# Performance work log

Measured on AMD Instinct MI355X. Metric: run time of the kernel, lower is better.

## Reference

```python
import jax, jax.numpy as jnp
import numpy as np

B = 32768
NM = 3      # number of modalities (len(mk))
NE = 8      # number of experts
D_IN = 768
D_P = 128   # per-modality projection dim
D_X = D_P * NM  # 384, concatenated feature dim


def setup_inputs() -> dict:
    key = jax.random.key(0)
    ks = jax.random.split(key, 16)
    s = 0.02
    return {
        "feat_text": jax.random.normal(ks[0], (B, D_IN), jnp.float32),
        "feat_audio": jax.random.normal(ks[1], (B, D_IN), jnp.float32),
        "feat_video": jax.random.normal(ks[2], (B, D_IN), jnp.float32),
        "proj_w": jax.random.normal(ks[3], (NM, D_IN, D_P), jnp.float32) * s,
        "proj_b": jax.random.normal(ks[4], (NM, D_P), jnp.float32) * s,
        "exp_w1": jax.random.normal(ks[5], (NE, D_X, D_P), jnp.float32) * s,
        "exp_b1": jax.random.normal(ks[6], (NE, D_P), jnp.float32) * s,
        "exp_w2": jax.random.normal(ks[7], (NE, D_P, D_P), jnp.float32) * s,
        "exp_b2": jax.random.normal(ks[8], (NE, D_P), jnp.float32) * s,
        "gate_w": jax.random.normal(ks[9], (D_X, NE), jnp.float32) * s,
        "gate_b": jax.random.normal(ks[10], (NE,), jnp.float32) * s,
        "pre_w": jax.random.normal(ks[11], (D_P, 64), jnp.float32) * s,
        "pre_b": jax.random.normal(ks[12], (64,), jnp.float32) * s,
        "head_w": jax.random.normal(ks[13], (64, 2), jnp.float32) * s,
        "head_b": jax.random.normal(ks[14], (2,), jnp.float32) * s,
    }


def reference(feat_text, feat_audio, feat_video, proj_w, proj_b,
              exp_w1, exp_b1, exp_w2, exp_b2, gate_w, gate_b,
              pre_w, pre_b, head_w, head_b):
    feats = jnp.stack([feat_text, feat_audio, feat_video], axis=0)  # [M,B,768]
    # per-modality projections, then concat: [B, 128*M]
    proj = jnp.einsum('mbd,mdp->mbp', feats, proj_w) + proj_b[:, None, :]
    x = jnp.concatenate(jnp.split(proj, NM, axis=0), axis=-1)[0]  # [B, 384]
    # gate: softmax over 8 experts
    gw = jax.nn.softmax(x @ gate_w + gate_b, axis=-1)  # [B, 8]
    # all experts as batched GEMM: [E,B,128]
    h = jax.nn.relu(jnp.einsum('bx,exh->ebh', x, exp_w1) + exp_b1[:, None, :])
    eo = jnp.einsum('ebh,eho->ebo', h, exp_w2) + exp_b2[:, None, :]
    fused = jnp.einsum('be,ebh->bh', gw, eo)  # weighted sum over experts
    penult = jax.nn.relu(fused @ pre_w + pre_b)  # Dropout is identity in eval
    logits = penult @ head_w + head_b  # [B, 2]
    return logits
```

## Files before the change

kernel.cpp:

```cpp
#include <hip/hip_runtime.h>
#include <hip/hip_bf16.h>

#define B_ROWS 32768

typedef unsigned short u16;
typedef unsigned int u32;
typedef float f32x4 __attribute__((ext_vector_type(4)));
typedef __bf16 bf16x8 __attribute__((ext_vector_type(8)));

__device__ __forceinline__ u16 f2bf(float f){
    union { float f; u32 u; } v; v.f = f;
    return (u16)((v.u + 0x7FFFu + ((v.u >> 16) & 1u)) >> 16);
}
__device__ __forceinline__ float bf2f(u16 h){
    union { u32 u; float f; } v; v.u = ((u32)h) << 16; return v.f;
}
__device__ __forceinline__ u32 cvtpk(float lo, float hi){
    u32 r;
    asm("v_cvt_pk_bf16_f32 %0, %1, %2" : "=v"(r) : "v"(lo), "v"(hi));
    return r;
}
__device__ __forceinline__ void async_cp16(void* lds_dst, const void* g_src){
    __builtin_amdgcn_global_load_lds(
        (const __attribute__((address_space(1))) unsigned int*)g_src,
        (__attribute__((address_space(3))) unsigned int*)lds_dst, 16, 0, 0);
}

__global__ void cast_weights_kernel(const float* __restrict__ proj_w,
                                    const float* __restrict__ exp_w1,
                                    const float* __restrict__ exp_w2,
                                    const float* __restrict__ pre_w,
                                    const float* __restrict__ gate_w,
                                    u16* __restrict__ pimg, u16* __restrict__ w1img,
                                    u16* __restrict__ w2img, u16* __restrict__ prwT,
                                    u16* __restrict__ gwimg){
    int i = blockIdx.x * 256 + threadIdx.x;
    if (i < 294912){
        int m = i / 98304, r = i % 98304;
        int c = r / 4096, rr = r % 4096;
        int col = rr >> 5, kk = rr & 31;
        int kb = kk ^ (((col >> 1) & 3) << 3);
        pimg[i] = f2bf(proj_w[m*98304 + (c*32 + kb)*128 + col]);
    } else if (i < 688128){
        int j = i - 294912;
        int e = j / 49152, r = j % 49152;
        int ph = r / 4096, rr = r % 4096;
        int q = rr >> 10, col = (rr >> 3) & 127, el = rr & 7;
        w1img[j] = f2bf(exp_w1[e*49152 + (ph*32 + q*8 + el)*128 + col]);
    } else if (i < 819200){
        int j = i - 688128;
        int e = j / 16384, r = j % 16384;
        int c2 = r / 4096, rr = r % 4096;
        int q = rr >> 10, col = (rr >> 3) & 127, el = rr & 7;
        w2img[j] = f2bf(exp_w2[e*16384 + (c2*32 + q*8 + el)*128 + col]);
    } else if (i < 827392){
        int j = i - 819200;
        int o = j / 128, k = j % 128;
        prwT[j] = f2bf(pre_w[k*64 + o]);
    } else if (i < 833536){
        int j = i - 827392;
        int e = j / 384, k = j % 384;
        gwimg[j] = (e < 8) ? f2bf(gate_w[k*8 + e]) : (u16)0;
    }
}

#define XS_OFF   0
#define ST_OFF   98304
#define WB_OFF   98304
#define HS_OFF   114688
#define GWT_OFF  149504
#define B1_OFF   153600
#define B2_OFF   155648

__global__ __launch_bounds__(512, 2) void fused_kernel(
    const float* __restrict__ ft, const float* __restrict__ fa, const float* __restrict__ fv,
    const u16* __restrict__ pimg, const float* __restrict__ proj_b,
    const u16* __restrict__ w1img, const u16* __restrict__ w2img,
    const u16* __restrict__ prwT, const u16* __restrict__ gwimg,
    const float* __restrict__ gate_b, const float* __restrict__ exp_b1, const float* __restrict__ exp_b2,
    const float* __restrict__ pre_b, const float* __restrict__ head_w, const float* __restrict__ head_b,
    float* __restrict__ out)
{
    __shared__ __align__(16) char lds[157696];
    const int tid = threadIdx.x;
    const int lane = tid & 63, wid = tid >> 6;
    const int wr = wid >> 1, wc = wid & 1;
    const int lr = lane & 15, q = lane >> 4;
    const int blk = blockIdx.x;
    const int row0 = blk * 128;
    const char* w1b = (const char*)w1img;
    const char* w2b = (const char*)w2img;
    u16* Hs  = (u16*)(lds + HS_OFF);
    u16* b1L = (u16*)(lds + B1_OFF);
    u16* b2L = (u16*)(lds + B2_OFF);

    if (tid < 384) ((float*)(lds + GWT_OFF))[tid] = proj_b[tid];
    for (int i = tid; i < 1024; i += 512){
        b1L[i] = f2bf(exp_b1[i]);
        b2L[i] = f2bf(exp_b2[i]);
    }
    asm volatile("s_waitcnt vmcnt(0)" ::: "memory");

    u32 aoffs[2];
    #pragma unroll
    for (int i = 0; i < 2; i++){
        int P = i*8192 + tid*16;
        int row = P >> 7, inner = P & 127;
        aoffs[i] = (u32)((row0 + row)*3072 + (inner ^ ((row & 7) << 4)));
    }

#define PSTAGE(s, c) do{                                                       \
        int mm = (c) / 24, kk = (c) % 24;                                      \
        const float* fb = (mm == 0) ? ft : (mm == 1) ? fa : fv;                \
        const char* ab = (const char*)fb;                                      \
        char* la = lds + ST_OFF + (s)*24576 + tid*16;                          \
        async_cp16(la,        ab + aoffs[0] + kk*128);                         \
        async_cp16(la + 8192, ab + aoffs[1] + kk*128);                         \
        async_cp16(lds + ST_OFF + (s)*24576 + 16384 + tid*16,                  \
                   (const char*)pimg + mm*196608 + kk*8192 + tid*16);          \
    }while(0)

#define PCONSUME(s) do{                                                        \
        const char* Abuf = lds + ST_OFF + (s)*24576;                           \
        const char* Bbuf = Abuf + 16384;                                       \
        bf16x8 af[2];                                                          \
        _Pragma("unroll")                                                      \
        for (int mi = 0; mi < 2; mi++){                                        \
            int row = wr*32 + mi*16 + lr;                                      \
            int aoff = row*128 + ((q*32) ^ ((row & 7) << 4));                  \
            f32x4 a0 = *(const f32x4*)(Abuf + aoff);                           \
            f32x4 a1 = *(const f32x4*)(Abuf + (aoff ^ 16));                    \
            union { u32 w[4]; bf16x8 v; } u;                                   \
            u.w[0] = cvtpk(a0.x, a0.y); u.w[1] = cvtpk(a0.z, a0.w);            \
            u.w[2] = cvtpk(a1.x, a1.y); u.w[3] = cvtpk(a1.z, a1.w);            \
            af[mi] = u.v;                                                      \
        }                                                                      \
        _Pragma("unroll")                                                      \
        for (int ni = 0; ni < 4; ni++){                                        \
            int col = wc*64 + ni*16 + lr;                                      \
            int boff = col*64 + ((q*16) ^ (((col >> 1) & 3) << 4));            \
            bf16x8 bf = *(const bf16x8*)(Bbuf + boff);                         \
            acc[0][ni] = __builtin_amdgcn_mfma_f32_16x16x32_bf16(af[0], bf, acc[0][ni], 0, 0, 0); \
            acc[1][ni] = __builtin_amdgcn_mfma_f32_16x16x32_bf16(af[1], bf, acc[1][ni], 0, 0, 0); \
        }                                                                      \
    }while(0)

    f32x4 acc[2][4];
    #pragma unroll
    for (int i = 0; i < 2; i++)
        #pragma unroll
        for (int j = 0; j < 4; j++) acc[i][j] = {0.f, 0.f, 0.f, 0.f};

    PSTAGE(0, 0);
    int cur = 0;
    #pragma unroll 1
    for (int m = 0; m < 3; m++){
        #pragma unroll 1
        for (int kt = 0; kt < 24; kt++){
            int t = m*24 + kt;
            __builtin_amdgcn_sched_barrier(0);
            __builtin_amdgcn_s_barrier();
            if (t < 71){
                PSTAGE(cur ^ 1, t + 1);
                asm volatile("s_waitcnt vmcnt(3)" ::: "memory");
            } else {
                asm volatile("s_waitcnt vmcnt(0)" ::: "memory");
            }
            __builtin_amdgcn_s_barrier();
            __builtin_amdgcn_sched_barrier(0);
            PCONSUME(cur);
            cur ^= 1;
        }
        const float* pbL = (const float*)(lds + GWT_OFF);
        #pragma unroll
        for (int mi = 0; mi < 2; mi++)
            #pragma unroll
            for (int ni = 0; ni < 4; ni++){
                int lcol = wc*64 + ni*16 + lr;
                int colg = m*128 + lcol;
                int ktI = colg >> 5, qI = (colg >> 3) & 3, el = colg & 7;
                float bias = pbL[m*128 + lcol];
                #pragma unroll
                for (int j = 0; j < 4; j++){
                    int row = wr*32 + mi*16 + q*4 + j;
                    *(u16*)(lds + (row >> 6)*49152 + ktI*4096 + qI*1024
                            + (row & 63)*16 + el*2) = f2bf(acc[mi][ni][j] + bias);
                    acc[mi][ni][j] = 0.f;
                }
            }
    }
#undef PSTAGE
#undef PCONSUME
    asm volatile("s_waitcnt lgkmcnt(0)" ::: "memory");
    __builtin_amdgcn_sched_barrier(0);
    __builtin_amdgcn_s_barrier();

    async_cp16(lds + WB_OFF + tid*16, w1b + tid*16);

    {
        f32x4 ga = {0.f, 0.f, 0.f, 0.f};
        const char* xb = lds + (wid >> 2)*49152 + ((wid & 3)*16 + lr)*16 + q*1024;
        const u16* gwp = gwimg + lr*384 + q*8;
        #pragma unroll
        for (int kt = 0; kt < 12; kt++){
            bf16x8 af = *(const bf16x8*)(xb + kt*4096);
            bf16x8 gb = *(const bf16x8*)(gwp + kt*32);
            ga = __builtin_amdgcn_mfma_f32_16x16x32_bf16(af, gb, ga, 0, 0, 0);
        }
        float gbv = gate_b[lr & 7];
        float gw4[4];
        #pragma unroll
        for (int j = 0; j < 4; j++){
            float v = ga[j] + gbv;
            float mx = v;
            mx = fmaxf(mx, __shfl_xor(mx, 1));
            mx = fmaxf(mx, __shfl_xor(mx, 2));
            mx = fmaxf(mx, __shfl_xor(mx, 4));
            float s = __expf(v - mx);
            float t = s;
            t += __shfl_xor(t, 1);
            t += __shfl_xor(t, 2);
            t += __shfl_xor(t, 4);
            gw4[j] = s / t;
        }
        __builtin_amdgcn_s_barrier();
        if (lr < 8){
            f32x4 wv = {gw4[0], gw4[1], gw4[2], gw4[3]};
            *(f32x4*)(lds + GWT_OFF + lr*512 + (wid*16 + q*4)*4) = wv;
        }
    }
    asm volatile("s_waitcnt vmcnt(0) lgkmcnt(0)" ::: "memory");
    __builtin_amdgcn_sched_barrier(0);
    __builtin_amdgcn_s_barrier();

    f32x4 fus[2][4];
    #pragma unroll
    for (int i = 0; i < 2; i++)
        #pragma unroll
        for (int j = 0; j < 4; j++) fus[i][j] = {0.f, 0.f, 0.f, 0.f};
    cur = 0;

    #pragma unroll 1
    for (int e = 0; e < 8; e++){
        f32x4 ac1[2][4];
        #pragma unroll
        for (int i = 0; i < 2; i++)
            #pragma unroll
            for (int j = 0; j < 4; j++) ac1[i][j] = {0.f, 0.f, 0.f, 0.f};

        #pragma unroll 1
        for (int ph = 0; ph < 12; ph++){
            __builtin_amdgcn_sched_barrier(0);
            __builtin_amdgcn_s_barrier();
            {
                int gn = e*16 + ph + 1;
                int en = gn >> 4, pn = gn & 15;
                const char* src = (pn < 12) ? (w1b + en*98304 + pn*8192)
                                            : (w2b + en*32768 + (pn - 12)*8192);
                async_cp16(lds + WB_OFF + (cur ^ 1)*8192 + tid*16, src + tid*16);
            }
            asm volatile("s_waitcnt vmcnt(1)" ::: "memory");
            __builtin_amdgcn_s_barrier();
            __builtin_amdgcn_sched_barrier(0);
            const char* wsl = lds + WB_OFF + cur*8192 + q*2048;
            const char* xa  = lds + (wr >> 1)*49152 + ph*4096 + q*1024;
            bf16x8 af0 = *(const bf16x8*)(xa + ((wr & 1)*32 + lr)*16);
            bf16x8 af1 = *(const bf16x8*)(xa + ((wr & 1)*32 + 16 + lr)*16);
            #pragma unroll
            for (int ni = 0; ni < 4; ni++){
                bf16x8 bf = *(const bf16x8*)(wsl + (wc*64 + ni*16 + lr)*16);
                ac1[0][ni] = __builtin_amdgcn_mfma_f32_16x16x32_bf16(af0, bf, ac1[0][ni], 0, 0, 0);
                ac1[1][ni] = __builtin_amdgcn_mfma_f32_16x16x32_bf16(af1, bf, ac1[1][ni], 0, 0, 0);
            }
            cur ^= 1;
        }
        #pragma unroll
        for (int mi = 0; mi < 2; mi++)
            #pragma unroll
            for (int ni = 0; ni < 4; ni++){
                int col = wc*64 + ni*16 + lr;
                float b1v = bf2f(b1L[e*128 + col]);
                #pragma unroll
                for (int j = 0; j < 4; j++){
                    int row = wr*32 + mi*16 + q*4 + j;
                    Hs[row*136 + col] = f2bf(fmaxf(ac1[mi][ni][j] + b1v, 0.f));
                }
            }
        asm volatile("s_waitcnt lgkmcnt(0)" ::: "memory");
        __builtin_amdgcn_sched_barrier(0);

        f32x4 ac2[2][4];
        #pragma unroll
        for (int i = 0; i < 2; i++)
            #pragma unroll
            for (int j = 0; j < 4; j++) ac2[i][j] = {0.f, 0.f, 0.f, 0.f};

        #pragma unroll 1
        for (int p2 = 0; p2 < 4; p2++){
            __builtin_amdgcn_sched_barrier(0);
            __builtin_amdgcn_s_barrier();
            {
                int gn = e*16 + 13 + p2;
                if (gn > 127) gn = 127;
                int en = gn >> 4, pn = gn & 15;
                const char* src = (pn < 12) ? (w1b + en*98304 + pn*8192)
                                            : (w2b + en*32768 + (pn - 12)*8192);
                async_cp16(lds + WB_OFF + (cur ^ 1)*8192 + tid*16, src + tid*16);
            }
            asm volatile("s_waitcnt vmcnt(1)" ::: "memory");
            __builtin_amdgcn_s_barrier();
            __builtin_amdgcn_sched_barrier(0);
            const char* wsl = lds + WB_OFF + cur*8192 + q*2048;
            const char* hb  = (const char*)Hs + (p2*32 + q*8)*2;
            bf16x8 af0 = *(const bf16x8*)(hb + (wr*32 + lr)*272);
            bf16x8 af1 = *(const bf16x8*)(hb + (wr*32 + 16 + lr)*272);
            #pragma unroll
            for (int ni = 0; ni < 4; ni++){
                bf16x8 bf = *(const bf16x8*)(wsl + (wc*64 + ni*16 + lr)*16);
                ac2[0][ni] = __builtin_amdgcn_mfma_f32_16x16x32_bf16(af0, bf, ac2[0][ni], 0, 0, 0);
                ac2[1][ni] = __builtin_amdgcn_mfma_f32_16x16x32_bf16(af1, bf, ac2[1][ni], 0, 0, 0);
            }
            cur ^= 1;
        }
        #pragma unroll
        for (int mi = 0; mi < 2; mi++){
            f32x4 gwv = *(const f32x4*)(lds + GWT_OFF + e*512 + (wr*32 + mi*16 + q*4)*4);
            #pragma unroll
            for (int ni = 0; ni < 4; ni++){
                int col = wc*64 + ni*16 + lr;
                float b2v = bf2f(b2L[e*128 + col]);
                #pragma unroll
                for (int j = 0; j < 4; j++)
                    fus[mi][ni][j] += gwv[j] * (ac2[mi][ni][j] + b2v);
            }
        }
    }

    asm volatile("s_waitcnt vmcnt(0)" ::: "memory");
    __builtin_amdgcn_sched_barrier(0);
    __builtin_amdgcn_s_barrier();
    #pragma unroll
    for (int mi = 0; mi < 2; mi++)
        #pragma unroll
        for (int ni = 0; ni < 4; ni++){
            int col = wc*64 + ni*16 + lr;
            #pragma unroll
            for (int j = 0; j < 4; j++){
                int row = wr*32 + mi*16 + q*4 + j;
                Hs[row*136 + col] = f2bf(fus[mi][ni][j]);
            }
        }
    asm volatile("s_waitcnt lgkmcnt(0)" ::: "memory");
    __builtin_amdgcn_sched_barrier(0);
    __builtin_amdgcn_s_barrier();

    f32x4 ap[4];
    #pragma unroll
    for (int i = 0; i < 4; i++) ap[i] = {0.f, 0.f, 0.f, 0.f};
    #pragma unroll
    for (int kt = 0; kt < 4; kt++){
        bf16x8 af = *(const bf16x8*)((const char*)Hs + (wid*16 + lr)*272 + (kt*32 + q*8)*2);
        #pragma unroll
        for (int ni = 0; ni < 4; ni++){
            bf16x8 bf = *(const bf16x8*)(prwT + (size_t)(ni*16 + lr)*128 + kt*32 + q*8);
            ap[ni] = __builtin_amdgcn_mfma_f32_16x16x32_bf16(af, bf, ap[ni], 0, 0, 0);
        }
    }
    float* Pen = (float*)lds;
    #pragma unroll
    for (int ni = 0; ni < 4; ni++){
        int col = ni*16 + lr;
        float pbv = pre_b[col];
        #pragma unroll
        for (int j = 0; j < 4; j++){
            int row = wid*16 + q*4 + j;
            Pen[row*68 + col] = fmaxf(ap[ni][j] + pbv, 0.f);
        }
    }
    asm volatile("s_waitcnt lgkmcnt(0)" ::: "memory");
    __builtin_amdgcn_sched_barrier(0);
    __builtin_amdgcn_s_barrier();
    if (tid < 256){
        int r = tid >> 1, c = tid & 1;
        float s = head_b[c];
        #pragma unroll 8
        for (int k = 0; k < 64; k++) s += Pen[r*68 + k] * head_w[k*2 + c];
        out[(size_t)(blk*128 + r)*2 + c] = s;
    }
}

extern "C" void kernel_launch(void* const* d_in, const int* in_sizes, int n_in,
                              void* d_out, int out_size, void* d_ws, size_t ws_size,
                              hipStream_t stream) {
    const float* ft     = (const float*)d_in[0];
    const float* fa     = (const float*)d_in[1];
    const float* fv     = (const float*)d_in[2];
    const float* proj_w = (const float*)d_in[3];
    const float* proj_b = (const float*)d_in[4];
    const float* exp_w1 = (const float*)d_in[5];
    const float* exp_b1 = (const float*)d_in[6];
    const float* exp_w2 = (const float*)d_in[7];
    const float* exp_b2 = (const float*)d_in[8];
    const float* gate_w = (const float*)d_in[9];
    const float* gate_b = (const float*)d_in[10];
    const float* pre_w  = (const float*)d_in[11];
    const float* pre_b  = (const float*)d_in[12];
    const float* head_w = (const float*)d_in[13];
    const float* head_b = (const float*)d_in[14];
    float* out = (float*)d_out;

    u16* pimg  = (u16*)d_ws;
    u16* w1img = pimg + 294912;
    u16* w2img = w1img + 393216;
    u16* prwT  = w2img + 131072;
    u16* gwimg = prwT + 8192;

    cast_weights_kernel<<<3256, 256, 0, stream>>>(proj_w, exp_w1, exp_w2, pre_w, gate_w,
                                                  pimg, w1img, w2img, prwT, gwimg);
    fused_kernel<<<256, 512, 0, stream>>>(ft, fa, fv, pimg, proj_b,
                                          w1img, w2img, prwT, gwimg,
                                          gate_b, exp_b1, exp_b2,
                                          pre_b, head_w, head_b, out);
}
```

Measured before the change: 122.6 us.

## Deepen async load pipelines to three stages and swizzle hidden-activation LDS layout

The projection GEMM now uses separate A and B staging buffers, with a triple-buffered A ring prefetched two steps ahead and a double-buffered B ring. The expert-weight stream is triple-buffered with a two-ahead prefetch, waiting on vmcnt(2) instead of vmcnt(1). The hidden-activation buffer switches from a padded 136-element stride to an XOR-swizzled 256-byte stride, and projection biases move into registers. LDS use grows to 160 KB, which may limit occupancy despite launch_bounds(512,2).

```diff
diff --git a/kernel.cpp b/kernel.cpp
--- a/kernel.cpp
+++ b/kernel.cpp
@@ -65,12 +65,13 @@
 }
 
 #define XS_OFF   0
-#define ST_OFF   98304
-#define WB_OFF   98304
-#define HS_OFF   114688
-#define GWT_OFF  149504
-#define B1_OFF   153600
-#define B2_OFF   155648
+#define A_OFF    98304
+#define B_OFF    147456
+#define HS_OFF   98304
+#define GWT_OFF  131072
+#define B1_OFF   135168
+#define B2_OFF   137216
+#define WB_OFF   139264
 
 __global__ __launch_bounds__(512, 2) void fused_kernel(
     const float* __restrict__ ft, const float* __restrict__ fa, const float* __restrict__ fv,
@@ -81,7 +82,7 @@
     const float* __restrict__ pre_b, const float* __restrict__ head_w, const float* __restrict__ head_b,
     float* __restrict__ out)
 {
-    __shared__ __align__(16) char lds[157696];
+    __shared__ __align__(16) char lds[163840];
     const int tid = threadIdx.x;
     const int lane = tid & 63, wid = tid >> 6;
     const int wr = wid >> 1, wc = wid & 1;
@@ -90,14 +91,17 @@
     const int row0 = blk * 128;
     const char* w1b = (const char*)w1img;
     const char* w2b = (const char*)w2img;
-    u16* Hs  = (u16*)(lds + HS_OFF);
+    char* HsB = lds + HS_OFF;
     u16* b1L = (u16*)(lds + B1_OFF);
     u16* b2L = (u16*)(lds + B2_OFF);
 
-    if (tid < 384) ((float*)(lds + GWT_OFF))[tid] = proj_b[tid];
-    for (int i = tid; i < 1024; i += 512){
-        b1L[i] = f2bf(exp_b1[i]);
-        b2L[i] = f2bf(exp_b2[i]);
+    float pb0[4], pb1[4], pb2[4];
+    #pragma unroll
+    for (int ni = 0; ni < 4; ni++){
+        int c = wc*64 + ni*16 + lr;
+        pb0[ni] = proj_b[c];
+        pb1[ni] = proj_b[128 + c];
+        pb2[ni] = proj_b[256 + c];
     }
     asm volatile("s_waitcnt vmcnt(0)" ::: "memory");
 
@@ -109,20 +113,23 @@
         aoffs[i] = (u32)((row0 + row)*3072 + (inner ^ ((row & 7) << 4)));
     }
 
-#define PSTAGE(s, c) do{                                                       \
-        int mm = (c) / 24, kk = (c) % 24;                                      \
-        const float* fb = (mm == 0) ? ft : (mm == 1) ? fa : fv;                \
-        const char* ab = (const char*)fb;                                      \
-        char* la = lds + ST_OFF + (s)*24576 + tid*16;                          \
-        async_cp16(la,        ab + aoffs[0] + kk*128);                         \
-        async_cp16(la + 8192, ab + aoffs[1] + kk*128);                         \
-        async_cp16(lds + ST_OFF + (s)*24576 + 16384 + tid*16,                  \
-                   (const char*)pimg + mm*196608 + kk*8192 + tid*16);          \
+#define ASTAGE(c) do{                                                          \
+        int mm_ = (c) / 24, kk_ = (c) % 24;                                    \
+        const char* ab_ = (const char*)(mm_ == 0 ? ft : mm_ == 1 ? fa : fv);   \
+        char* la_ = lds + A_OFF + ((c) % 3)*16384 + tid*16;                    \
+        async_cp16(la_,        ab_ + aoffs[0] + kk_*128);                      \
+        async_cp16(la_ + 8192, ab_ + aoffs[1] + kk_*128);                      \
     }while(0)
 
-#define PCONSUME(s) do{                                                        \
-        const char* Abuf = lds + ST_OFF + (s)*24576;                           \
-        const char* Bbuf = Abuf + 16384;                                       \
+#define BSTAGE(c) do{                                                          \
+        int mm_ = (c) / 24, kk_ = (c) % 24;                                    \
+        async_cp16(lds + B_OFF + ((c) % 2)*8192 + tid*16,                      \
+                   (const char*)pimg + mm_*196608 + kk_*8192 + tid*16);        \
+    }while(0)
+
+#define PCONSUME(c) do{                                                        \
+        const char* Abuf = lds + A_OFF + ((c) % 3)*16384;                      \
+        const char* Bbuf = lds + B_OFF + ((c) % 2)*8192;                       \
         bf16x8 af[2];                                                          \
         _Pragma("unroll")                                                      \
         for (int mi = 0; mi < 2; mi++){                                        \
@@ -145,58 +152,63 @@
         }                                                                      \
     }while(0)
 
+#define PHASE_A_MOD(MC, PB) do{                                                \
+        _Pragma("unroll 1")                                                    \
+        for (int kt = 0; kt < 24; kt++){                                       \
+            int t = MC*24 + kt;                                                \
+            __builtin_amdgcn_sched_barrier(0);                                 \
+            __builtin_amdgcn_s_barrier();                                      \
+            if (t < 71) BSTAGE(t + 1);                                         \
+            if (t < 70) ASTAGE(t + 2);                                         \
+            if (t < 70)       asm volatile("s_waitcnt vmcnt(5)" ::: "memory"); \
+            else if (t == 70) asm volatile("s_waitcnt vmcnt(3)" ::: "memory"); \
+            else              asm volatile("s_waitcnt vmcnt(0)" ::: "memory"); \
+            __builtin_amdgcn_s_barrier();                                      \
+            __builtin_amdgcn_sched_barrier(0);                                 \
+            PCONSUME(t);                                                       \
+        }                                                                      \
+        _Pragma("unroll")                                                      \
+        for (int mi = 0; mi < 2; mi++)                                         \
+            _Pragma("unroll")                                                  \
+            for (int ni = 0; ni < 4; ni++){                                    \
+                int lcol = wc*64 + ni*16 + lr;                                 \
+                int colg = MC*128 + lcol;                                      \
+                int ktI = colg >> 5, qI = (colg >> 3) & 3, el = colg & 7;      \
+                _Pragma("unroll")                                              \
+                for (int j = 0; j < 4; j++){                                   \
+                    int row = wr*32 + mi*16 + q*4 + j;                         \
+                    *(u16*)(lds + (row >> 6)*49152 + ktI*4096 + qI*1024        \
+                            + (row & 63)*16 + el*2) = f2bf(acc[mi][ni][j] + PB[ni]); \
+                    acc[mi][ni][j] = 0.f;                                      \
+                }                                                              \
+            }                                                                  \
+    }while(0)
+
     f32x4 acc[2][4];
     #pragma unroll
     for (int i = 0; i < 2; i++)
         #pragma unroll
         for (int j = 0; j < 4; j++) acc[i][j] = {0.f, 0.f, 0.f, 0.f};
 
-    PSTAGE(0, 0);
-    int cur = 0;
-    #pragma unroll 1
-    for (int m = 0; m < 3; m++){
-        #pragma unroll 1
-        for (int kt = 0; kt < 24; kt++){
-            int t = m*24 + kt;
-            __builtin_amdgcn_sched_barrier(0);
-            __builtin_amdgcn_s_barrier();
-            if (t < 71){
-                PSTAGE(cur ^ 1, t + 1);
-                asm volatile("s_waitcnt vmcnt(3)" ::: "memory");
-            } else {
-                asm volatile("s_waitcnt vmcnt(0)" ::: "memory");
-            }
-            __builtin_amdgcn_s_barrier();
-            __builtin_amdgcn_sched_barrier(0);
-            PCONSUME(cur);
-            cur ^= 1;
-        }
-        const float* pbL = (const float*)(lds + GWT_OFF);
-        #pragma unroll
-        for (int mi = 0; mi < 2; mi++)
-            #pragma unroll
-            for (int ni = 0; ni < 4; ni++){
-                int lcol = wc*64 + ni*16 + lr;
-                int colg = m*128 + lcol;
-                int ktI = colg >> 5, qI = (colg >> 3) & 3, el = colg & 7;
-                float bias = pbL[m*128 + lcol];
-                #pragma unroll
-                for (int j = 0; j < 4; j++){
-                    int row = wr*32 + mi*16 + q*4 + j;
-                    *(u16*)(lds + (row >> 6)*49152 + ktI*4096 + qI*1024
-                            + (row & 63)*16 + el*2) = f2bf(acc[mi][ni][j] + bias);
-                    acc[mi][ni][j] = 0.f;
-                }
-            }
-    }
-#undef PSTAGE
+    BSTAGE(0); ASTAGE(0); ASTAGE(1);
+    PHASE_A_MOD(0, pb0);
+    PHASE_A_MOD(1, pb1);
+    PHASE_A_MOD(2, pb2);
+#undef ASTAGE
+#undef BSTAGE
 #undef PCONSUME
+#undef PHASE_A_MOD
+
     asm volatile("s_waitcnt lgkmcnt(0)" ::: "memory");
     __builtin_amdgcn_sched_barrier(0);
     __builtin_amdgcn_s_barrier();
 
-    async_cp16(lds + WB_OFF + tid*16, w1b + tid*16);
-
+    async_cp16(lds + WB_OFF + 0*8192 + tid*16, w1b + tid*16);
+    async_cp16(lds + WB_OFF + 1*8192 + tid*16, w1b + 8192 + tid*16);
+    for (int i = tid; i < 1024; i += 512){
+        b1L[i] = f2bf(exp_b1[i]);
+        b2L[i] = f2bf(exp_b2[i]);
+    }
     {
         f32x4 ga = {0.f, 0.f, 0.f, 0.f};
         const char* xb = lds + (wid >> 2)*49152 + ((wid & 3)*16 + lr)*16 + q*1024;
@@ -223,7 +235,6 @@
             t += __shfl_xor(t, 4);
             gw4[j] = s / t;
         }
-        __builtin_amdgcn_s_barrier();
         if (lr < 8){
             f32x4 wv = {gw4[0], gw4[1], gw4[2], gw4[3]};
             *(f32x4*)(lds + GWT_OFF + lr*512 + (wid*16 + q*4)*4) = wv;
@@ -233,12 +244,19 @@
     __builtin_amdgcn_sched_barrier(0);
     __builtin_amdgcn_s_barrier();
 
+#define WSTAGE(g) do{                                                          \
+        int gn_ = (g) > 127 ? 127 : (g);                                       \
+        int en_ = gn_ >> 4, pn_ = gn_ & 15;                                    \
+        const char* src_ = (pn_ < 12) ? (w1b + en_*98304 + pn_*8192)           \
+                                      : (w2b + en_*32768 + (pn_ - 12)*8192);   \
+        async_cp16(lds + WB_OFF + ((g) % 3)*8192 + tid*16, src_ + tid*16);     \
+    }while(0)
+
     f32x4 fus[2][4];
     #pragma unroll
     for (int i = 0; i < 2; i++)
         #pragma unroll
         for (int j = 0; j < 4; j++) fus[i][j] = {0.f, 0.f, 0.f, 0.f};
-    cur = 0;
 
     #pragma unroll 1
     for (int e = 0; e < 8; e++){
@@ -250,19 +268,14 @@
 
         #pragma unroll 1
         for (int ph = 0; ph < 12; ph++){
+            int g = e*16 + ph;
             __builtin_amdgcn_sched_barrier(0);
             __builtin_amdgcn_s_barrier();
-            {
-                int gn = e*16 + ph + 1;
-                int en = gn >> 4, pn = gn & 15;
-                const char* src = (pn < 12) ? (w1b + en*98304 + pn*8192)
-                                            : (w2b + en*32768 + (pn - 12)*8192);
-                async_cp16(lds + WB_OFF + (cur ^ 1)*8192 + tid*16, src + tid*16);
-            }
-            asm volatile("s_waitcnt vmcnt(1)" ::: "memory");
+            WSTAGE(g + 2);
+            asm volatile("s_waitcnt vmcnt(2)" ::: "memory");
             __builtin_amdgcn_s_barrier();
             __builtin_amdgcn_sched_barrier(0);
-            const char* wsl = lds + WB_OFF + cur*8192 + q*2048;
+            const char* wsl = lds + WB_OFF + (g % 3)*8192 + q*2048;
             const char* xa  = lds + (wr >> 1)*49152 + ph*4096 + q*1024;
             bf16x8 af0 = *(const bf16x8*)(xa + ((wr & 1)*32 + lr)*16);
             bf16x8 af1 = *(const bf16x8*)(xa + ((wr & 1)*32 + 16 + lr)*16);
@@ -272,7 +285,6 @@
                 ac1[0][ni] = __builtin_amdgcn_mfma_f32_16x16x32_bf16(af0, bf, ac1[0][ni], 0, 0, 0);
                 ac1[1][ni] = __builtin_amdgcn_mfma_f32_16x16x32_bf16(af1, bf, ac1[1][ni], 0, 0, 0);
             }
-            cur ^= 1;
         }
         #pragma unroll
         for (int mi = 0; mi < 2; mi++)
@@ -283,7 +295,8 @@
                 #pragma unroll
                 for (int j = 0; j < 4; j++){
                     int row = wr*32 + mi*16 + q*4 + j;
-                    Hs[row*136 + col] = f2bf(fmaxf(ac1[mi][ni][j] + b1v, 0.f));
+                    *(u16*)(HsB + row*256 + ((col*2) ^ ((row & 7) << 4)))
+                        = f2bf(fmaxf(ac1[mi][ni][j] + b1v, 0.f));
                 }
             }
         asm volatile("s_waitcnt lgkmcnt(0)" ::: "memory");
@@ -297,30 +310,25 @@
 
         #pragma unroll 1
         for (int p2 = 0; p2 < 4; p2++){
+            int g = e*16 + 12 + p2;
             __builtin_amdgcn_sched_barrier(0);
             __builtin_amdgcn_s_barrier();
-            {
-                int gn = e*16 + 13 + p2;
-                if (gn > 127) gn = 127;
-                int en = gn >> 4, pn = gn & 15;
-                const char* src = (pn < 12) ? (w1b + en*98304 + pn*8192)
-                                            : (w2b + en*32768 + (pn - 12)*8192);
-                async_cp16(lds + WB_OFF + (cur ^ 1)*8192 + tid*16, src + tid*16);
-            }
-            asm volatile("s_waitcnt vmcnt(1)" ::: "memory");
+            WSTAGE(g + 2);
+            asm volatile("s_waitcnt vmcnt(2)" ::: "memory");
             __builtin_amdgcn_s_barrier();
             __builtin_amdgcn_sched_barrier(0);
-            const char* wsl = lds + WB_OFF + cur*8192 + q*2048;
-            const char* hb  = (const char*)Hs + (p2*32 + q*8)*2;
-            bf16x8 af0 = *(const bf16x8*)(hb + (wr*32 + lr)*272);
-            bf16x8 af1 = *(const bf16x8*)(hb + (wr*32 + 16 + lr)*272);
+            const char* wsl = lds + WB_OFF + (g % 3)*8192 + q*2048;
+            int cb = p2*64 + q*16;
+            int rowA = wr*32 + lr;
+            int rowB = wr*32 + 16 + lr;
+            bf16x8 af0 = *(const bf16x8*)(HsB + rowA*256 + (cb ^ ((rowA & 7) << 4)));
+            bf16x8 af1 = *(const bf16x8*)(HsB + rowB*256 + (cb ^ ((rowB & 7) << 4)));
             #pragma unroll
             for (int ni = 0; ni < 4; ni++){
                 bf16x8 bf = *(const bf16x8*)(wsl + (wc*64 + ni*16 + lr)*16);
                 ac2[0][ni] = __builtin_amdgcn_mfma_f32_16x16x32_bf16(af0, bf, ac2[0][ni], 0, 0, 0);
                 ac2[1][ni] = __builtin_amdgcn_mfma_f32_16x16x32_bf16(af1, bf, ac2[1][ni], 0, 0, 0);
             }
-            cur ^= 1;
         }
         #pragma unroll
         for (int mi = 0; mi < 2; mi++){
@@ -335,6 +343,7 @@
             }
         }
     }
+#undef WSTAGE
 
     asm volatile("s_waitcnt vmcnt(0)" ::: "memory");
     __builtin_amdgcn_sched_barrier(0);
@@ -347,7 +356,7 @@
             #pragma unroll
             for (int j = 0; j < 4; j++){
                 int row = wr*32 + mi*16 + q*4 + j;
-                Hs[row*136 + col] = f2bf(fus[mi][ni][j]);
+                *(u16*)(HsB + row*256 + ((col*2) ^ ((row & 7) << 4))) = f2bf(fus[mi][ni][j]);
             }
         }
     asm volatile("s_waitcnt lgkmcnt(0)" ::: "memory");
@@ -359,7 +368,9 @@
     for (int i = 0; i < 4; i++) ap[i] = {0.f, 0.f, 0.f, 0.f};
     #pragma unroll
     for (int kt = 0; kt < 4; kt++){
-        bf16x8 af = *(const bf16x8*)((const char*)Hs + (wid*16 + lr)*272 + (kt*32 + q*8)*2);
+        int row = wid*16 + lr;
+        int cb = kt*64 + q*16;
+        bf16x8 af = *(const bf16x8*)(HsB + row*256 + (cb ^ ((row & 7) << 4)));
         #pragma unroll
         for (int ni = 0; ni < 4; ni++){
             bf16x8 bf = *(const bf16x8*)(prwT + (size_t)(ni*16 + lr)*128 + kt*32 + q*8);
```

After: 121.0 us. Within noise of the previous version (-1.3%).
